# Kernel optimization log

Hardware: AMD Instinct MI355X
Metric: run time of the kernel (lower is better)

Reference implementation:

```python
import jax, jax.numpy as jnp
import numpy as np

N_NODES = 10000


def gcn_conv(x, W, b, src, dst, num_nodes):
    """PyG GCNConv: add self-loops, symmetric deg^{-1/2} normalization,
    linear transform (no bias in lin), scatter-add aggregation, then bias."""
    xw = x @ W  # (N, H)
    # degree on A + I (self-loops added)
    deg = jnp.zeros((num_nodes,), dtype=x.dtype).at[dst].add(1.0) + 1.0
    dinv = jax.lax.rsqrt(deg)  # (N,)
    norm = dinv[src] * dinv[dst]  # (E,)
    msg = xw[src] * norm[:, None]  # (E, H) gathered messages
    agg = jax.ops.segment_sum(msg, dst, num_segments=num_nodes)
    # self-loop contribution: norm_ii = dinv_i^2
    agg = agg + xw * (dinv * dinv)[:, None]
    return agg + b


def setup_inputs() -> dict:
    key = jax.random.key(0)
    k1, k2, k3, k4 = jax.random.split(key, 4)
    N, F, H, E = N_NODES, 256, 512, 320000
    x = jax.random.normal(k1, (N, F), dtype=jnp.float32)
    edge_index = jax.random.randint(k2, (2, E), 0, N, dtype=jnp.int64)
    W1 = jax.random.normal(k3, (F, H), dtype=jnp.float32) * (1.0 / np.sqrt(F))
    b1 = jnp.zeros((H,), dtype=jnp.float32)
    W2 = jax.random.normal(k4, (H, F), dtype=jnp.float32) * (1.0 / np.sqrt(H))
    b2 = jnp.zeros((F,), dtype=jnp.float32)
    return {"x": x, "edge_index": edge_index, "W1": W1, "b1": b1, "W2": W2, "b2": b2}


def reference(x, edge_index, W1, b1, W2, b2):
    src, dst = edge_index[0], edge_index[1]
    h = jax.nn.relu(gcn_conv(x, W1, b1, src, dst, N_NODES))
    h = jax.nn.relu(gcn_conv(h, W2, b2, src, dst, N_NODES))
    # global_max_pool with single graph (batch all zeros) -> (1, F)
    return jnp.max(h, axis=0, keepdims=True)
```

## Files before the change

### kernel.cpp

```cpp
#include <hip/hip_runtime.h>

#define NNODES 10000
#define MP 10112
#define F 256
#define H 512
#define CAP 128

typedef _Float16 half8 __attribute__((ext_vector_type(8)));
typedef float floatx4 __attribute__((ext_vector_type(4)));
typedef float floatx8 __attribute__((ext_vector_type(8)));

__global__ __launch_bounds__(256) void prep_k(const float* __restrict__ W1,
                                              const float* __restrict__ W2,
                                              const float* __restrict__ x,
                                              _Float16* __restrict__ W1t,
                                              _Float16* __restrict__ W2t,
                                              _Float16* __restrict__ xh,
                                              int* __restrict__ cnt) {
  int gt = blockIdx.x * 256 + threadIdx.x;
  if (gt < NNODES) cnt[gt] = 0;
  if (gt < H * F) {
    W1t[gt] = (_Float16)W1[(gt & 255) * H + (gt >> 8)];
    W2t[gt] = (_Float16)W2[(gt & 511) * F + (gt >> 9)];
  }
  if (gt < NNODES * F / 8) {
    floatx8 v = *(const floatx8*)(x + (size_t)gt * 8);
    *(half8*)(xh + (size_t)gt * 8) = __builtin_convertvector(v, half8);
  }
}

__global__ __launch_bounds__(256) void build_k(const int* __restrict__ src,
                                               const int* __restrict__ dst,
                                               int* __restrict__ cnt,
                                               int* __restrict__ csr, int E) {
  int e = blockIdx.x * blockDim.x + threadIdx.x;
  if (e < E) {
    int d = dst[e];
    int p = atomicAdd(&cnt[d], 1);
    if (p < CAP) csr[(size_t)d * CAP + p] = src[e];
  }
}

template <bool FUSE_MAX>
__global__ __launch_bounds__(256) void aggb_k(const _Float16* __restrict__ in,
                                              const int* __restrict__ cnt,
                                              const int* __restrict__ csr,
                                              const float* __restrict__ bias,
                                              _Float16* __restrict__ outh,
                                              float* __restrict__ out) {
  __shared__ float smem[2048];
  int tid = threadIdx.x;
  int lane = tid & 63, wvi = tid >> 6;
  int half = lane >> 5, hl = lane & 31;
  int f0 = hl * 8;
  int node = (blockIdx.x * 4 + wvi) * 2 + half;
  floatx8 bb = {};
  if (FUSE_MAX) bb = *(const floatx8*)(bias + f0);
  floatx8 lmax = {};
  {
    int deg = min(cnt[node], CAP);
    float di = rsqrtf((float)(deg + 1));
    const int* bucket = csr + (size_t)node * CAP;
    floatx8 acc = {};
    for (int c = 0; c < deg; c += 32) {
      int m = min(32, deg - c);
      int sv = 0; float wvv = 0.f;
      if (hl < m) {
        sv = bucket[c + hl];
        wvv = rsqrtf((float)(cnt[sv] + 1));
      }
      int j = 0;
      for (; j + 8 <= m; j += 8) {
        #pragma unroll
        for (int u = 0; u < 8; u++) {
          int sj = __shfl(sv, (half << 5) | (j + u), 64);
          float wj = __shfl(wvv, (half << 5) | (j + u), 64);
          half8 hv = *(const half8*)(in + (size_t)sj * F + f0);
          acc += wj * __builtin_convertvector(hv, floatx8);
        }
      }
      for (; j < m; j++) {
        int sj = __shfl(sv, (half << 5) | j, 64);
        float wj = __shfl(wvv, (half << 5) | j, 64);
        half8 hv = *(const half8*)(in + (size_t)sj * F + f0);
        acc += wj * __builtin_convertvector(hv, floatx8);
      }
    }
    half8 xsv = *(const half8*)(in + (size_t)node * F + f0);
    floatx8 tot = di * acc + (di * di) * __builtin_convertvector(xsv, floatx8);
    if (FUSE_MAX) {
      tot += bb;
      #pragma unroll
      for (int t = 0; t < 8; t++) lmax[t] = fmaxf(lmax[t], fmaxf(tot[t], 0.f));
    } else {
      *(half8*)(outh + (size_t)node * F + f0) = __builtin_convertvector(tot, half8);
    }
  }
  if (FUSE_MAX) {
    float* srow = smem + (size_t)(wvi * 2 + half) * 256;
    *(floatx8*)(srow + f0) = lmax;
    __syncthreads();
    float m = smem[tid];
    #pragma unroll
    for (int r = 1; r < 8; r++) m = fmaxf(m, smem[r * 256 + tid]);
    atomicMax((int*)&out[tid], __float_as_int(m));
  }
}

template <int K, int NT, int NJ, bool RELU>
__global__ __launch_bounds__(256) void gemm_k(const _Float16* __restrict__ A,
                                              const _Float16* __restrict__ Bt,
                                              const float* __restrict__ bias,
                                              _Float16* __restrict__ C) {
  int lane = threadIdx.x & 63;
  int wv = threadIdx.x >> 6;
  int r = lane & 15, q = lane >> 4;
  int m0 = blockIdx.x * 128 + (wv & 1) * 64;
  int n0 = blockIdx.y * (2 * NJ * 16) + (wv >> 1) * (NJ * 16);
  floatx4 acc[4][NJ] = {};
  const _Float16* Ap = A + (size_t)(m0 + r) * K + q * 8;
  const _Float16* Bp = Bt + (size_t)(n0 + r) * K + q * 8;
  for (int k0 = 0; k0 < K; k0 += 32) {
    half8 a[4], bb[NJ];
    #pragma unroll
    for (int i = 0; i < 4; i++) a[i] = *(const half8*)(Ap + (size_t)i * 16 * K + k0);
    #pragma unroll
    for (int j = 0; j < NJ; j++) bb[j] = *(const half8*)(Bp + (size_t)j * 16 * K + k0);
    #pragma unroll
    for (int i = 0; i < 4; i++)
      #pragma unroll
      for (int j = 0; j < NJ; j++)
        acc[i][j] = __builtin_amdgcn_mfma_f32_16x16x32_f16(a[i], bb[j], acc[i][j], 0, 0, 0);
  }
  #pragma unroll
  for (int i = 0; i < 4; i++) {
    #pragma unroll
    for (int j = 0; j < NJ; j++) {
      int n = n0 + j * 16 + r;
      float bv = RELU ? bias[n] : 0.f;
      #pragma unroll
      for (int rr = 0; rr < 4; rr++) {
        int row = m0 + i * 16 + q * 4 + rr;
        float v = acc[i][j][rr] + bv;
        if (RELU) v = fmaxf(v, 0.f);
        C[(size_t)row * NT + n] = (_Float16)v;
      }
    }
  }
}

extern "C" void kernel_launch(void* const* d_in, const int* in_sizes, int n_in,
                              void* d_out, int out_size, void* d_ws, size_t ws_size,
                              hipStream_t stream) {
  const float* x  = (const float*)d_in[0];
  const int*   ei = (const int*)d_in[1];
  const float* W1 = (const float*)d_in[2];
  const float* b1 = (const float*)d_in[3];
  const float* W2 = (const float*)d_in[4];
  const float* b2 = (const float*)d_in[5];
  const int E = in_sizes[1] / 2;
  const int N = NNODES;
  const int* src = ei;
  const int* dst = ei + E;

  char* w = (char*)d_ws;
  size_t off = 0;
  auto take = [&](size_t bytes) -> void* {
    void* p = w + off;
    off += (bytes + 255) & ~(size_t)255;
    return p;
  };
  int*       cnt    = (int*)take((size_t)N * 4);
  int*       csr    = (int*)take((size_t)N * CAP * 4);
  _Float16*  W1t    = (_Float16*)take((size_t)H * F * 2);
  _Float16*  W2t    = (_Float16*)take((size_t)F * H * 2);
  _Float16*  xh     = (_Float16*)take((size_t)N * F * 2);
  _Float16*  axh    = (_Float16*)take((size_t)MP * F * 2);
  _Float16*  h1h    = (_Float16*)take((size_t)MP * H * 2);
  _Float16*  xw2h   = (_Float16*)take((size_t)MP * F * 2);

  prep_k<<<1280, 256, 0, stream>>>(W1, W2, x, W1t, W2t, xh, cnt);
  build_k<<<(E + 255) / 256, 256, 0, stream>>>(src, dst, cnt, csr, E);
  aggb_k<false><<<1250, 256, 0, stream>>>(xh, cnt, csr, nullptr, axh, nullptr);
  gemm_k<F, H, 4, true><<<dim3(MP / 128, 4), 256, 0, stream>>>(axh, W1t, b1, h1h);
  gemm_k<H, F, 2, false><<<dim3(MP / 128, 4), 256, 0, stream>>>(h1h, W2t, nullptr, xw2h);
  aggb_k<true><<<1250, 256, 0, stream>>>(xw2h, cnt, csr, b2, nullptr, (float*)d_out);
}
```

Measured before the change: 196.6 us.

## Fuse both dense GEMMs into one kernel with the hidden tile kept in LDS

Replaces the two separate GEMM launches with one kernel. Each block computes a 32-row tile of relu(A·W1+b1) into padded shared memory, then multiplies that tile by W2 straight from LDS. This removes one launch and the global write and read of the 10112x512 fp16 hidden activation. In exchange, every block rereads the full W1t and W2t from cache, the row tile is smaller, and each block uses about 33KB of LDS. The prep grid shrinks to exactly cover the element count.

New measurement: 187.2 us. -4.8%, faster.

```diff
diff --git a/kernel.cpp b/kernel.cpp
--- a/kernel.cpp
+++ b/kernel.cpp
@@ -5,6 +5,7 @@
 #define F 256
 #define H 512
 #define CAP 128
+#define H1STR 520
 
 typedef _Float16 half8 __attribute__((ext_vector_type(8)));
 typedef float floatx4 __attribute__((ext_vector_type(4)));
@@ -107,43 +108,75 @@
   }
 }
 
-template <int K, int NT, int NJ, bool RELU>
-__global__ __launch_bounds__(256) void gemm_k(const _Float16* __restrict__ A,
-                                              const _Float16* __restrict__ Bt,
-                                              const float* __restrict__ bias,
-                                              _Float16* __restrict__ C) {
+__global__ __launch_bounds__(256) void gemm12_k(const _Float16* __restrict__ A,
+                                                const _Float16* __restrict__ W1t,
+                                                const float* __restrict__ b1,
+                                                const _Float16* __restrict__ W2t,
+                                                _Float16* __restrict__ C) {
+  __shared__ _Float16 h1[32 * H1STR];
   int lane = threadIdx.x & 63;
   int wv = threadIdx.x >> 6;
   int r = lane & 15, q = lane >> 4;
-  int m0 = blockIdx.x * 128 + (wv & 1) * 64;
-  int n0 = blockIdx.y * (2 * NJ * 16) + (wv >> 1) * (NJ * 16);
-  floatx4 acc[4][NJ] = {};
-  const _Float16* Ap = A + (size_t)(m0 + r) * K + q * 8;
-  const _Float16* Bp = Bt + (size_t)(n0 + r) * K + q * 8;
-  for (int k0 = 0; k0 < K; k0 += 32) {
-    half8 a[4], bb[NJ];
+  int m0 = blockIdx.x * 32;
+
+  {
+    floatx4 acc[2][8] = {};
+    const _Float16* Ap = A + (size_t)(m0 + r) * F + q * 8;
+    const _Float16* Bp = W1t + (size_t)(wv * 128 + r) * F + q * 8;
+    for (int k0 = 0; k0 < F; k0 += 32) {
+      half8 a[2], b[8];
+      #pragma unroll
+      for (int i = 0; i < 2; i++) a[i] = *(const half8*)(Ap + (size_t)i * 16 * F + k0);
+      #pragma unroll
+      for (int j = 0; j < 8; j++) b[j] = *(const half8*)(Bp + (size_t)j * 16 * F + k0);
+      #pragma unroll
+      for (int i = 0; i < 2; i++)
+        #pragma unroll
+        for (int j = 0; j < 8; j++)
+          acc[i][j] = __builtin_amdgcn_mfma_f32_16x16x32_f16(a[i], b[j], acc[i][j], 0, 0, 0);
+    }
     #pragma unroll
-    for (int i = 0; i < 4; i++) a[i] = *(const half8*)(Ap + (size_t)i * 16 * K + k0);
+    for (int i = 0; i < 2; i++) {
+      #pragma unroll
+      for (int j = 0; j < 8; j++) {
+        int n = wv * 128 + j * 16 + r;
+        float bv = b1[n];
+        #pragma unroll
+        for (int rr = 0; rr < 4; rr++) {
+          int row = i * 16 + q * 4 + rr;
+          h1[row * H1STR + n] = (_Float16)fmaxf(acc[i][j][rr] + bv, 0.f);
+        }
+      }
+    }
+  }
+  __syncthreads();
+
+  {
+    floatx4 acc[2][4] = {};
+    const _Float16* Bp = W2t + (size_t)(wv * 64 + r) * H + q * 8;
+    for (int k0 = 0; k0 < H; k0 += 32) {
+      half8 a[2], b[4];
+      #pragma unroll
+      for (int i = 0; i < 2; i++)
+        a[i] = *(const half8*)(h1 + (i * 16 + r) * H1STR + k0 + q * 8);
+      #pragma unroll
+      for (int j = 0; j < 4; j++) b[j] = *(const half8*)(Bp + (size_t)j * 16 * H + k0);
+      #pragma unroll
+      for (int i = 0; i < 2; i++)
+        #pragma unroll
+        for (int j = 0; j < 4; j++)
+          acc[i][j] = __builtin_amdgcn_mfma_f32_16x16x32_f16(a[i], b[j], acc[i][j], 0, 0, 0);
+    }
     #pragma unroll
-    for (int j = 0; j < NJ; j++) bb[j] = *(const half8*)(Bp + (size_t)j * 16 * K + k0);
-    #pragma unroll
-    for (int i = 0; i < 4; i++)
-      #pragma unroll
-      for (int j = 0; j < NJ; j++)
-        acc[i][j] = __builtin_amdgcn_mfma_f32_16x16x32_f16(a[i], bb[j], acc[i][j], 0, 0, 0);
-  }
-  #pragma unroll
-  for (int i = 0; i < 4; i++) {
-    #pragma unroll
-    for (int j = 0; j < NJ; j++) {
-      int n = n0 + j * 16 + r;
-      float bv = RELU ? bias[n] : 0.f;
-      #pragma unroll
-      for (int rr = 0; rr < 4; rr++) {
-        int row = m0 + i * 16 + q * 4 + rr;
-        float v = acc[i][j][rr] + bv;
-        if (RELU) v = fmaxf(v, 0.f);
-        C[(size_t)row * NT + n] = (_Float16)v;
+    for (int i = 0; i < 2; i++) {
+      #pragma unroll
+      for (int j = 0; j < 4; j++) {
+        int n = wv * 64 + j * 16 + r;
+        #pragma unroll
+        for (int rr = 0; rr < 4; rr++) {
+          int row = m0 + i * 16 + q * 4 + rr;
+          C[(size_t)row * F + n] = (_Float16)acc[i][j][rr];
+        }
       }
     }
   }
@@ -176,13 +209,11 @@
   _Float16*  W2t    = (_Float16*)take((size_t)F * H * 2);
   _Float16*  xh     = (_Float16*)take((size_t)N * F * 2);
   _Float16*  axh    = (_Float16*)take((size_t)MP * F * 2);
-  _Float16*  h1h    = (_Float16*)take((size_t)MP * H * 2);
   _Float16*  xw2h   = (_Float16*)take((size_t)MP * F * 2);
 
-  prep_k<<<1280, 256, 0, stream>>>(W1, W2, x, W1t, W2t, xh, cnt);
+  prep_k<<<1250, 256, 0, stream>>>(W1, W2, x, W1t, W2t, xh, cnt);
   build_k<<<(E + 255) / 256, 256, 0, stream>>>(src, dst, cnt, csr, E);
   aggb_k<false><<<1250, 256, 0, stream>>>(xh, cnt, csr, nullptr, axh, nullptr);
-  gemm_k<F, H, 4, true><<<dim3(MP / 128, 4), 256, 0, stream>>>(axh, W1t, b1, h1h);
-  gemm_k<H, F, 2, false><<<dim3(MP / 128, 4), 256, 0, stream>>>(h1h, W2t, nullptr, xw2h);
+  gemm12_k<<<MP / 32, 256, 0, stream>>>(axh, W1t, b1, W2t, xw2h);
   aggb_k<true><<<1250, 256, 0, stream>>>(xw2h, cnt, csr, b2, nullptr, (float*)d_out);
 }
```
